# Performance work log

Hardware: AMD Instinct MI355X
Metric: run time of the kernel (lower is better)

The kernel has to match this reference:

```python
import jax, jax.numpy as jnp
import numpy as np

B, T, V, E, H, M, U, W = 8, 64, 30000, 256, 512, 512, 32, 512


def setup_inputs():
    rng = np.random.RandomState(0)
    ks = jax.random.split(jax.random.key(0), 20)
    u_len = rng.randint(U // 2, U + 1, size=B).astype(np.int32)
    w_len = rng.randint(W // 2, W + 1, size=B).astype(np.int32)
    # word2utt[b, j] = utterance index owning word j; padded words -> last valid utt
    w2u = np.zeros((B, W), np.int32)
    for b in range(B):
        j = np.minimum(np.arange(W), w_len[b] - 1)
        w2u[b] = np.minimum((j * u_len[b]) // w_len[b], u_len[b] - 1)
    s = 0.02
    p = lambda i, shp: jax.random.normal(ks[i], shp, jnp.float32) * s
    emb = p(0, (V, E)).at[0].set(0.0)  # padding_idx=0
    return {
        'target': jax.random.randint(ks[1], (B, T), 0, V, jnp.int32),
        'u_output': jax.random.normal(ks[2], (B, U, M), jnp.float32),
        'w_output': jax.random.normal(ks[3], (B, W, M), jnp.float32),
        'u_len': jnp.asarray(u_len), 'w_len': jnp.asarray(w_len), 'word2utt': jnp.asarray(w2u),
        'emb': emb,
        'W_ih': p(4, (3 * H, E)), 'W_hh': p(5, (3 * H, H)),
        'b_ih': p(6, (3 * H,)), 'b_hh': p(7, (3 * H,)),
        'Wu': p(8, (H, M)), 'bu': p(9, (H,)),
        'Ww': p(10, (H, M)), 'bw': p(11, (H,)),
        'Wo': p(12, (V, H + M)), 'bo': p(13, (V,)),
        'Wd': p(14, (1, V)), 'Wy': p(15, (1, E)),
        'Ws': p(16, (1, H)), 'bs': p(17, (1,)),
    }


def reference(target, u_output, w_output, u_len, w_len, word2utt,
              emb, W_ih, W_hh, b_ih, b_hh, Wu, bu, Ww, bw, Wo, bo, Wd, Wy, Ws, bs):
    Bn = target.shape[0]
    Un = u_output.shape[1]
    Vn = Wo.shape[0]
    Au = jnp.einsum('bum,hm->buh', u_output, Wu) + bu  # attention_u(u_output)
    Aw = jnp.einsum('bwm,hm->bwh', w_output, Ww) + bw  # attention_w(w_output)
    u_mask = jnp.arange(Un)[None, :] < u_len[:, None]               # [B,U]
    w_mask = jnp.arange(w_output.shape[1])[None, :] < w_len[:, None]  # [B,W]
    # initial hidden = last valid utterance state (mem_hidden == dec_hidden)
    h0 = jnp.take_along_axis(u_output, (u_len - 1)[:, None, None], axis=1)[:, 0, :]

    def gru_step(x, h):
        gi = x @ W_ih.T + b_ih
        gh = h @ W_hh.T + b_hh
        ir, iz, inn = jnp.split(gi, 3, axis=-1)
        hr, hz, hn = jnp.split(gh, 3, axis=-1)
        r = jax.nn.sigmoid(ir + hr)
        z = jax.nn.sigmoid(iz + hz)
        n = jnp.tanh(inn + r * hn)
        return (1.0 - z) * n + z * h

    def seg_softmax(sw, seg, valid):  # per-batch ragged per-utterance softmax over words
        swm = jnp.where(valid, sw, -jnp.inf)
        m = jax.ops.segment_max(swm, seg, num_segments=Un)
        e = jnp.where(valid, jnp.exp(sw - m[seg]), 0.0)
        d = jax.ops.segment_sum(e, seg, num_segments=Un)
        return e / d[seg]

    def step(carry, yt):
        h, d_prev, eu_prev = carry
        y = emb[yt]                               # [B,E]
        h_new = gru_step(y, h)                    # rnn_output == new hidden (1 layer)
        su = jnp.einsum('bh,buh->bu', h_new, Au)
        su = jax.nn.softmax(jnp.where(u_mask, su, -jnp.inf), axis=-1)
        gamma = jax.nn.sigmoid(d_prev @ Wd.T + y @ Wy.T + h_new @ Ws.T + bs)  # [B,1]
        su = (1.0 - gamma) * su + gamma * eu_prev
        su = su / jnp.sum(su, axis=-1, keepdims=True)
        sw = jnp.einsum('bh,bwh->bw', h_new, Aw)
        pw = jax.vmap(seg_softmax)(sw, word2utt, w_mask)        # [B,W]
        suw = jnp.take_along_axis(su, word2utt, axis=1) * pw    # [B,W]
        ctx = jnp.einsum('bw,bwm->bm', suw, w_output)
        logits = jnp.concatenate([ctx, h_new], axis=-1) @ Wo.T + bo
        dt = jax.nn.log_softmax(logits, axis=-1)
        return (h_new, dt, su), (dt, suw, su)

    init = (h0, jnp.zeros((Bn, Vn), jnp.float32), jnp.zeros((Bn, Un), jnp.float32))
    _, (dts, suws, sus) = jax.lax.scan(step, init, target.T)
    dec_output = jnp.swapaxes(dts, 0, 1)   # [B,T,V]
    scores_uw = jnp.swapaxes(suws, 0, 1)   # [B,T,W]
    scores_u = jnp.swapaxes(sus, 0, 1)     # [B,T,U]
    return dec_output, scores_uw, scores_u
```

## Files before the change

### kernel.cpp

```cpp
#include <hip/hip_runtime.h>
#include <math.h>

typedef unsigned short ushort_t;
typedef unsigned int uint_t;
typedef unsigned long long ulong_t;
typedef __attribute__((ext_vector_type(8))) short s16x8;
typedef __attribute__((ext_vector_type(4))) float f32x4;

#define BB 8
#define TT 64
#define VV 30000
#define VP 30080
#define EE 256
#define HH 512
#define MM 512
#define UU 32
#define WW 512
#define G3 1536
#define NLB 235
#define NDB 235
#define NBG 64

#define OFF_GI    0
#define OFF_YALL  786432
#define OFF_WY    917504
#define OFF_H0    918016
#define OFF_HALL  922112
#define OFF_HU    1184256
#define OFF_HW    1446400
#define OFF_HS    1708544
#define OFF_HWV   1709056
#define OFF_P     1709568
#define OFF_SW    1725952
#define OFF_C     1988096
#define OFF_E     6182400
#define OFF_WV    6198784
#define OFF_PART  6204416
#define OFF_LSE   6208832
#define OFF_WOV   6209344
#define OFF_HBT   13909824
#define OFF_SYNC  14040896

#define DEC_SZ (BB*TT*VV)
#define SUW_OFF DEC_SZ
#define SU_OFF  (DEC_SZ + BB*TT*WW)

__device__ __forceinline__ float sigm(float x){ return 1.0f/(1.0f+__expf(-x)); }
__device__ __forceinline__ ushort_t to_bf16(float f){
  uint_t u = __float_as_uint(f);
  return (ushort_t)((u + 0x7fffu + ((u>>16)&1u)) >> 16);
}
__device__ __forceinline__ float from_bf16(ushort_t s){
  return __uint_as_float(((uint_t)s) << 16);
}


template<int TRANSB>
__global__ void __launch_bounds__(256)
k_gemm_b(const float* __restrict__ A, int lda, int aS,
         const float* __restrict__ B, int ldb, int bS,
         const float* __restrict__ bias,
         float* __restrict__ C, int ldc, int cS, int K){
  A += (size_t)blockIdx.z * aS;
  B += (size_t)blockIdx.z * bS;
  C += (size_t)blockIdx.z * cS;
  __shared__ float As[32][65];
  __shared__ float Bs[32][65];
  int tid = threadIdx.x;
  int bx = blockIdx.x, by = blockIdx.y;
  int tx = tid & 15, ty = tid >> 4;
  float acc[4][4] = {};
  for (int k0 = 0; k0 < K; k0 += 32){
    {
      int r = tid >> 2, cbase = (tid & 3) * 8;
      const float* ap = A + (size_t)(by*64 + r)*lda + k0 + cbase;
      #pragma unroll
      for (int i=0;i<8;++i) As[cbase+i][r] = ap[i];
    }
    if (TRANSB){
      int r = tid >> 2, cbase = (tid & 3) * 8;
      const float* bp = B + (size_t)(bx*64 + r)*ldb + k0 + cbase;
      #pragma unroll
      for (int i=0;i<8;++i) Bs[cbase+i][r] = bp[i];
    } else {
      int kk = tid >> 3, cbase = (tid & 7) * 8;
      const float* bp = B + (size_t)(k0 + kk)*ldb + bx*64 + cbase;
      #pragma unroll
      for (int i=0;i<8;++i) Bs[kk][cbase+i] = bp[i];
    }
    __syncthreads();
    #pragma unroll
    for (int kk=0;kk<32;++kk){
      float a0=As[kk][ty*4+0], a1=As[kk][ty*4+1], a2=As[kk][ty*4+2], a3=As[kk][ty*4+3];
      float b0=Bs[kk][tx*4+0], b1=Bs[kk][tx*4+1], b2=Bs[kk][tx*4+2], b3=Bs[kk][tx*4+3];
      acc[0][0]+=a0*b0; acc[0][1]+=a0*b1; acc[0][2]+=a0*b2; acc[0][3]+=a0*b3;
      acc[1][0]+=a1*b0; acc[1][1]+=a1*b1; acc[1][2]+=a1*b2; acc[1][3]+=a1*b3;
      acc[2][0]+=a2*b0; acc[2][1]+=a2*b1; acc[2][2]+=a2*b2; acc[2][3]+=a2*b3;
      acc[3][0]+=a3*b0; acc[3][1]+=a3*b1; acc[3][2]+=a3*b2; acc[3][3]+=a3*b3;
    }
    __syncthreads();
  }
  #pragma unroll
  for (int i=0;i<4;++i){
    int row = by*64 + ty*4 + i;
    #pragma unroll
    for (int j=0;j<4;++j){
      int col = bx*64 + tx*4 + j;
      float v = acc[i][j];
      if (bias) v += bias[col];
      C[(size_t)row*ldc + col] = v;
    }
  }
}

__global__ void k_gather_y(const int* __restrict__ target, const float* __restrict__ emb,
                           float* __restrict__ ws){
  int idx = blockIdx.x*256 + threadIdx.x;
  int bt = idx >> 8; int e = idx & 255;
  int tok = target[bt];
  ws[OFF_YALL + idx] = emb[tok*EE + e];
}

__global__ void k_wy(const float* __restrict__ Wy, float* __restrict__ ws){
  int wid  = blockIdx.x*4 + (threadIdx.x>>6);
  int lane = threadIdx.x & 63;
  const float* y = ws + OFF_YALL + wid*EE;
  float acc = 0.f;
  for (int e=lane; e<EE; e+=64) acc += y[e]*Wy[e];
  for (int off=32; off; off>>=1) acc += __shfl_xor(acc, off);
  if (lane == 0) ws[OFF_WY + wid] = acc;
}

__global__ void k_h0(const float* __restrict__ u_output, const int* __restrict__ u_len,
                     float* __restrict__ ws){
  int idx = blockIdx.x*256 + threadIdx.x;
  int b = idx >> 9; int k = idx & 511;
  int u = u_len[b]-1;
  ws[OFF_H0 + idx] = u_output[(b*UU+u)*MM + k];
}

__global__ void __launch_bounds__(256)
k_wovc(const float* __restrict__ Wo, ushort_t* __restrict__ wov){
  int idx8 = blockIdx.x*256 + threadIdx.x;
  int v = idx8 >> 6;
  int k8 = (idx8 & 63) << 3;
  uint_t u0=0,u1=0,u2=0,u3=0;
  if (v < VV){
    const float* src = Wo + (size_t)v*1024 + k8;
    float4 f0 = *(const float4*)src;
    float4 f1 = *(const float4*)(src+4);
    u0 = (uint_t)to_bf16(f0.x) | ((uint_t)to_bf16(f0.y) << 16);
    u1 = (uint_t)to_bf16(f0.z) | ((uint_t)to_bf16(f0.w) << 16);
    u2 = (uint_t)to_bf16(f1.x) | ((uint_t)to_bf16(f1.y) << 16);
    u3 = (uint_t)to_bf16(f1.z) | ((uint_t)to_bf16(f1.w) << 16);
  }
  uint4 pk = make_uint4(u0,u1,u2,u3);
  *(uint4*)(wov + (size_t)idx8*8) = pk;
}

__global__ void __launch_bounds__(256)
k_wv(const float* __restrict__ Wo, const float* __restrict__ bo,
     const float* __restrict__ Wd, float* __restrict__ wv){
  __shared__ float wds[128];
  __shared__ float red[256];
  int tid = threadIdx.x;
  int v0 = blockIdx.x*128;
  float pbo=0.f, pwd=0.f;
  if (tid < 128){
    int v = v0 + tid;
    float wd = (v<VV)? Wd[v] : 0.f;
    wds[tid] = wd;
    pbo = wd * ((v<VV)? bo[v] : 0.f);
    pwd = wd;
  }
  __syncthreads();
  float4 acc = {0,0,0,0};
  int nmax = (v0 + 128 <= VV) ? 128 : (VV - v0);
  for (int i=0;i<nmax;++i){
    float wd = wds[i];
    float4 w4 = *(const float4*)(Wo + (size_t)(v0+i)*1024 + tid*4);
    acc.x += wd*w4.x; acc.y += wd*w4.y; acc.z += wd*w4.z; acc.w += wd*w4.w;
  }
  atomicAdd(&wv[tid*4+0], acc.x);
  atomicAdd(&wv[tid*4+1], acc.y);
  atomicAdd(&wv[tid*4+2], acc.z);
  atomicAdd(&wv[tid*4+3], acc.w);
  red[tid] = pbo; __syncthreads();
  for (int s=128; s; s>>=1){ if (tid<s) red[tid]+=red[tid+s]; __syncthreads(); }
  if (tid==0) atomicAdd(&wv[1024], red[0]);
  __syncthreads();
  red[tid] = pwd; __syncthreads();
  for (int s=128; s; s>>=1){ if (tid<s) red[tid]+=red[tid+s]; __syncthreads(); }
  if (tid==0) atomicAdd(&wv[1025], red[0]);
}


__global__ void __launch_bounds__(512)
k_gru_persist(const float* __restrict__ W_hh, const float* __restrict__ b_hh,
              float* __restrict__ ws){
  uint_t* sy    = (uint_t*)(ws + OFF_SYNC);
  uint_t* flags = sy;
  uint_t* go    = sy + 4096;
  int k    = blockIdx.x*8 + (threadIdx.x>>6);
  int lane = threadIdx.x & 63;
  const float* gi_all = ws + OFF_GI;
  const float* wr = W_hh + (size_t)k*HH;
  const float* wz = W_hh + (size_t)(HH+k)*HH;
  const float* wn = W_hh + (size_t)(2*HH+k)*HH;
  float bhr = b_hh[k], bhz = b_hh[HH+k], bhn = b_hh[2*HH+k];

  for (int t=0; t<TT; ++t){
    const float* hin = (t==0) ? (ws+OFF_H0) : (ws+OFF_HALL + (size_t)(t-1)*4096);
    float* hout = ws + OFF_HALL + (size_t)t*4096;
    float pr[8], pz[8], pn[8];
    #pragma unroll
    for (int b=0;b<8;++b){ pr[b]=0.f; pz[b]=0.f; pn[b]=0.f; }
    #pragma unroll 2
    for (int kk=lane; kk<HH; kk+=64){
      float w1 = wr[kk], w2 = wz[kk], w3 = wn[kk];
      #pragma unroll
      for (int b=0;b<8;++b){
        float hv = hin[b*HH+kk];
        pr[b] += hv*w1; pz[b] += hv*w2; pn[b] += hv*w3;
      }
    }
    #pragma unroll
    for (int off=32; off; off>>=1){
      #pragma unroll
      for (int b=0;b<8;++b){
        pr[b] += __shfl_xor(pr[b],off);
        pz[b] += __shfl_xor(pz[b],off);
        pn[b] += __shfl_xor(pn[b],off);
      }
    }
    if (lane == 0){
      #pragma unroll
      for (int b=0;b<8;++b){
        const float* gi = gi_all + (b*TT + t)*G3;
        float r = sigm(gi[k]      + pr[b] + bhr);
        float z = sigm(gi[HH+k]   + pz[b] + bhz);
        float n = tanhf(gi[2*HH+k] + r*(pn[b] + bhn));
        hout[b*HH+k] = (1.f-z)*n + z*hin[b*HH+k];
      }
    }
    __syncthreads();
    if (threadIdx.x == 0)
      __hip_atomic_store(&flags[blockIdx.x*32], (uint_t)(t+1), __ATOMIC_RELEASE, __HIP_MEMORY_SCOPE_AGENT);
    if (blockIdx.x == 0){
      if ((int)threadIdx.x < NBG){
        while (__hip_atomic_load(&flags[threadIdx.x*32], __ATOMIC_RELAXED, __HIP_MEMORY_SCOPE_AGENT) < (uint_t)(t+1))
          __builtin_amdgcn_s_sleep(2);
      }
      __syncthreads();
      if (threadIdx.x == 0)
        __hip_atomic_store(go, (uint_t)(t+1), __ATOMIC_RELEASE, __HIP_MEMORY_SCOPE_AGENT);
    } else {
      if (threadIdx.x == 0){
        while (__hip_atomic_load(go, __ATOMIC_RELAXED, __HIP_MEMORY_SCOPE_AGENT) < (uint_t)(t+1))
          __builtin_amdgcn_s_sleep(2);
      }
    }
    __syncthreads();
  }
}


__global__ void k_hbt(const float* __restrict__ ws, ushort_t* __restrict__ hbt){
  int idx = blockIdx.x*256 + threadIdx.x;
  hbt[idx] = to_bf16(ws[OFF_HALL + idx]);
}

__global__ void __launch_bounds__(256)
k_lh_mfma(const float* __restrict__ Wo, const float* __restrict__ bo,
          const ushort_t* __restrict__ hbt, float* __restrict__ out){
  int tid = threadIdx.x;
  int wv = tid >> 6, l = tid & 63;
  int lm = l & 15, lg = l >> 4;
  int vbase = blockIdx.x*128 + wv*32;
  int rbase = blockIdx.y*128;
  f32x4 acc[2][8];
  #pragma unroll
  for (int s=0;s<2;++s)
    #pragma unroll
    for (int rt=0;rt<8;++rt) acc[s][rt] = (f32x4){0.f,0.f,0.f,0.f};

  for (int k0 = 0; k0 < 512; k0 += 32){
    int kk = k0 + lg*8;
    union { uint_t u[4]; s16x8 s; } af[2];
    #pragma unroll
    for (int s=0;s<2;++s){
      int v = vbase + s*16 + lm; if (v >= VV) v = VV-1;
      const float* ap = Wo + (size_t)v*1024 + 512 + kk;
      float4 f0 = *(const float4*)ap;
      float4 f1 = *(const float4*)(ap+4);
      af[s].u[0] = ((__float_as_uint(f0.x)+0x8000u)>>16) | ((__float_as_uint(f0.y)+0x8000u) & 0xffff0000u);
      af[s].u[1] = ((__float_as_uint(f0.z)+0x8000u)>>16) | ((__float_as_uint(f0.w)+0x8000u) & 0xffff0000u);
      af[s].u[2] = ((__float_as_uint(f1.x)+0x8000u)>>16) | ((__float_as_uint(f1.y)+0x8000u) & 0xffff0000u);
      af[s].u[3] = ((__float_as_uint(f1.z)+0x8000u)>>16) | ((__float_as_uint(f1.w)+0x8000u) & 0xffff0000u);
    }
    #pragma unroll
    for (int rt=0;rt<8;++rt){
      const ushort_t* bp = hbt + (size_t)(rbase + rt*16 + lm)*HH + kk;
      s16x8 bf = *(const s16x8*)bp;
      acc[0][rt] = __builtin_amdgcn_mfma_f32_16x16x32_bf16(af[0].s, bf, acc[0][rt], 0, 0, 0);
      acc[1][rt] = __builtin_amdgcn_mfma_f32_16x16x32_bf16(af[1].s, bf, acc[1][rt], 0, 0, 0);
    }
  }
  float bv[2][4];
  #pragma unroll
  for (int s=0;s<2;++s)
    #pragma unroll
    for (int r=0;r<4;++r){
      int v = vbase + s*16 + lg*4 + r;
      bv[s][r] = (v < VV) ? bo[v] : 0.f;
    }
  #pragma unroll
  for (int rt=0;rt<8;++rt){
    int row = rbase + rt*16 + lm;
    float* orow = out + (size_t)((row&7)*TT + (row>>3))*VV;
    #pragma unroll
    for (int s=0;s<2;++s){
      #pragma unroll
      for (int r=0;r<4;++r){
        int v = vbase + s*16 + lg*4 + r;
        if (v < VV) orow[v] = acc[s][rt][r] + bv[s][r];
      }
    }
  }
}


__global__ void k_hdots(const float* __restrict__ Ws, float* __restrict__ ws){
  int wid  = blockIdx.x*4 + (threadIdx.x>>6);
  int lane = threadIdx.x & 63;
  int row = wid >> 1, which = wid & 1;
  const float* h = ws + OFF_HALL + row*HH;
  const float* src = which ? (ws + OFF_WV + 512) : Ws;
  float acc = 0.f;
  for (int k=lane; k<HH; k+=64) acc += h[k]*src[k];
  for (int off=32; off; off>>=1) acc += __shfl_xor(acc, off);
  if (lane == 0) (which ? ws+OFF_HWV : ws+OFF_HS)[row] = acc;
}

__global__ void k_p(const float* __restrict__ u_output, const int* __restrict__ u_len,
                    float* __restrict__ ws){
  int row = blockIdx.x;
  int b = row & 7;
  int tid = threadIdx.x;
  __shared__ float su_s[UU];
  {
    int u = tid >> 3, l8 = tid & 7;
    const float* hu = ws + OFF_HU + row*512;
    const float* uo = u_output + (size_t)(b*UU + u)*MM;
    float acc = 0.f;
    for (int m=l8; m<MM; m+=8) acc += hu[m]*uo[m];
    acc += __shfl_xor(acc,1); acc += __shfl_xor(acc,2); acc += __shfl_xor(acc,4);
    if (l8 == 0) su_s[u] = acc;
  }
  __syncthreads();
  if (tid < 32){
    int ul = u_len[b];
    float sv = su_s[tid];
    bool valid = tid < ul;
    float mv = valid ? sv : -1e30f;
    for (int off=16; off; off>>=1) mv = fmaxf(mv, __shfl_xor(mv, off));
    float e = valid ? __expf(sv - mv) : 0.f;
    float ssum = e;
    for (int off=16; off; off>>=1) ssum += __shfl_xor(ssum, off);
    ws[OFF_P + row*UU + tid] = e/ssum;
  }
}

__global__ void k_pw(const int* __restrict__ word2utt, const int* __restrict__ w_len,
                     float* __restrict__ ws){
  int row = blockIdx.x;
  int b = row & 7;
  int tid = threadIdx.x;
  __shared__ float sarr[WW];
  __shared__ int   seg[WW];
  __shared__ float marr[UU], darr[UU];
  int wl = w_len[b];
  float* swrow = ws + OFF_SW + row*WW;
  for (int w=tid; w<WW; w+=256){ sarr[w] = swrow[w]; seg[w] = word2utt[b*WW+w]; }
  __syncthreads();
  {
    int g = tid>>3, l8 = tid&7;
    float mv = -1e30f;
    for (int w=l8; w<wl; w+=8) if (seg[w]==g) mv = fmaxf(mv, sarr[w]);
    mv = fmaxf(mv, __shfl_xor(mv,1)); mv = fmaxf(mv, __shfl_xor(mv,2)); mv = fmaxf(mv, __shfl_xor(mv,4));
    float d = 0.f;
    for (int w=l8; w<wl; w+=8) if (seg[w]==g) d += __expf(sarr[w]-mv);
    d += __shfl_xor(d,1); d += __shfl_xor(d,2); d += __shfl_xor(d,4);
    if (l8 == 0){ marr[g]=mv; darr[g]=d; }
  }
  __syncthreads();
  for (int w=tid; w<WW; w+=256){
    float val = 0.f;
    if (w < wl){ int u = seg[w]; val = __expf(sarr[w]-marr[u])/darr[u]; }
    swrow[w] = val;
  }
}

__global__ void __launch_bounds__(256)
k_C(const float* __restrict__ w_output, const int* __restrict__ w_len,
    const int* __restrict__ u_len, const int* __restrict__ word2utt,
    float* __restrict__ ws){
  int row = blockIdx.x;
  int b = row & 7;
  int tid = threadIdx.x;
  __shared__ float pws[WW];
  __shared__ int   seg[WW];
  __shared__ int   st[UU], en[UU];
  __shared__ float wvs[512];
  __shared__ float red4[8];
  int wl = w_len[b], ul = u_len[b];
  const float* pwrow = ws + OFF_SW + row*WW;
  for (int w=tid; w<WW; w+=256){ pws[w] = pwrow[w]; seg[w] = word2utt[b*WW+w]; }
  for (int m=tid; m<512; m+=256) wvs[m] = ws[OFF_WV + m];
  if (tid < UU){ st[tid]=0; en[tid]=0; }
  __syncthreads();
  for (int w=tid; w<wl; w+=256){
    int s = seg[w];
    if (w==0 || seg[w-1]!=s) st[s]=w;
    if (w==wl-1 || seg[w+1]!=s) en[s]=w+1;
  }
  __syncthreads();
  ushort_t* Cu = (ushort_t*)(ws + OFF_C);
  int m0 = tid, m1 = tid + 256;
  int lane = tid & 63, wvi = tid >> 6;
  for (int u=0; u<UU; ++u){
    float acc0=0.f, acc1=0.f;
    if (u < ul){
      int s = st[u], e = en[u];
      for (int w=s; w<e; ++w){
        float p = pws[w];
        const float* wo = w_output + ((size_t)(b*WW+w))*MM;
        acc0 += p*wo[m0];
        acc1 += p*wo[m1];
      }
    }
    size_t cbase = ((size_t)row*UU + u)*512;
    Cu[cbase + m0] = to_bf16(acc0);
    Cu[cbase + m1] = to_bf16(acc1);
    float part = acc0*wvs[m0] + acc1*wvs[m1];
    for (int off=32; off; off>>=1) part += __shfl_xor(part, off);
    if (lane == 0) red4[wvi] = part;
    __syncthreads();
    if (tid == 0) ws[OFF_E + row*UU + u] = red4[0]+red4[1]+red4[2]+red4[3];
    __syncthreads();
  }
}


__global__ void __launch_bounds__(256)
k_decode_persist(const int* __restrict__ u_len, const float* __restrict__ bs,
                 const ushort_t* __restrict__ wov,
                 float* __restrict__ ws, float* __restrict__ out){
  int bid = blockIdx.x;
  int tid = threadIdx.x;
  uint_t* sy    = (uint_t*)(ws + OFF_SYNC);
  uint_t* flags = sy + 8192;
  uint_t* go    = sy + 16000;
  __shared__ float suL[8][32];
  __shared__ float qbufL[8], lseL[8], gamL[8];
  __shared__ int   ulS[8];
  __shared__ uint_t cbU[16*260];
  __shared__ float2 wred[4][8];
  __shared__ float cst[4];
  if (tid == 0){ cst[0]=bs[0]; cst[1]=ws[OFF_WV+1024]; cst[2]=ws[OFF_WV+1025]; }
  if (tid < 8){ qbufL[tid]=0.f; lseL[tid]=0.f; ulS[tid]=u_len[tid]; }
  suL[tid>>5][tid&31] = 0.f;
  for (int i=tid; i<8*260; i+=256) cbU[8*260 + i] = 0u;
  __syncthreads();

  const ulong_t* partq = (const ulong_t*)(ws + OFF_PART);
  int wv = tid >> 6, l = tid & 63;
  int lm = l & 15, lgp = l >> 4;

  for (int t=0; t<TT; ++t){
    int b = tid >> 5, j = tid & 31;
    int row = t*8 + b;

    if (t > 0 && tid < 8)
      lseL[tid] = __hip_atomic_load((const float*)(ws + OFF_LSE + (t-1)*8 + tid),
                                    __ATOMIC_RELAXED, __HIP_MEMORY_SCOPE_AGENT);
    __syncthreads();
    if (tid < 8){
      float pd = 0.f;
      if (t > 0)
        pd = qbufL[tid] + ws[OFF_HWV + (t-1)*8 + tid] + cst[1] - lseL[tid]*cst[2];
      gamL[tid] = sigm(pd + ws[OFF_WY + tid*TT + t] + ws[OFF_HS + t*8 + tid] + cst[0]);
    }
    __syncthreads();
    {
      float gg = gamL[b];
      float p = ws[OFF_P + row*UU + j];
      float eu = suL[b][j];
      float mix = (1.f-gg)*p + gg*eu;
      float s2 = mix;
      #pragma unroll
      for (int off=16; off; off>>=1) s2 += __shfl_xor(s2, off);
      float su = mix / s2;
      suL[b][j] = su;
      float qp = su * ws[OFF_E + row*UU + j];
      #pragma unroll
      for (int off=16; off; off>>=1) qp += __shfl_xor(qp, off);
      if (j == 0) qbufL[b] = qp;
    }
    __syncthreads();
    if (bid < 8 && tid < 32)
      out[SU_OFF + (bid*TT + t)*UU + tid] = suL[bid][tid];
    {
      int m16 = j * 16;
      int ul = ulS[b];
      const ushort_t* Crow = (const ushort_t*)(ws + OFF_C) + ((size_t)row*UU)*512 + m16;
      float acc[16];
      #pragma unroll
      for (int i=0;i<16;++i) acc[i]=0.f;
      for (int u=0; u<ul; ++u){
        float su = suL[b][u];
        uint4 c0 = *(const uint4*)(Crow + (size_t)u*512);
        uint4 c1 = *(const uint4*)(Crow + (size_t)u*512 + 8);
        uint_t cc[8] = {c0.x,c0.y,c0.z,c0.w,c1.x,c1.y,c1.z,c1.w};
        #pragma unroll
        for (int q=0;q<8;++q){
          acc[2*q]   += su * __uint_as_float((cc[q] & 0xffffu) << 16);
          acc[2*q+1] += su * __uint_as_float((cc[q] >> 16) << 16);
        }
      }
      #pragma unroll
      for (int q=0;q<8;++q){
        uint_t pk = (uint_t)to_bf16(acc[2*q]) | ((uint_t)to_bf16(acc[2*q+1]) << 16);
        cbU[b*260 + j*8 + q] = pk;
      }
    }
    __syncthreads();

    {
      int v0w = bid*128 + wv*32;
      f32x4 acc0 = {0.f,0.f,0.f,0.f}, acc1 = {0.f,0.f,0.f,0.f};
      const ushort_t* ap0 = wov + (size_t)(v0w + lm)*512 + lgp*8;
      const ushort_t* ap1 = ap0 + 16*512;
      const uint_t* cbrow = cbU + lm*260 + lgp*4;
      #pragma unroll
      for (int ks=0; ks<16; ++ks){
        s16x8 av0 = *(const s16x8*)(ap0 + ks*32);
        s16x8 av1 = *(const s16x8*)(ap1 + ks*32);
        s16x8 bv  = *(const s16x8*)(cbrow + ks*16);
        acc0 = __builtin_amdgcn_mfma_f32_16x16x32_bf16(av0, bv, acc0, 0, 0, 0);
        acc1 = __builtin_amdgcn_mfma_f32_16x16x32_bf16(av1, bv, acc1, 0, 0, 0);
      }
      float pm = -1e30f, ps = 0.f;
      if (lm < 8){
        float* orow = out + ((size_t)(lm*TT + t))*VV;
        float l8v[8];
        #pragma unroll
        for (int vt=0; vt<2; ++vt){
          int vb = v0w + vt*16 + lgp*4;
          f32x4 a = vt ? acc1 : acc0;
          if (vb + 3 < VV){
            float4 o = *(const float4*)(orow + vb);
            float g0 = a[0]+o.x, g1 = a[1]+o.y, g2 = a[2]+o.z, g3 = a[3]+o.w;
            *(float4*)(orow + vb) = make_float4(g0,g1,g2,g3);
            l8v[vt*4+0]=g0; l8v[vt*4+1]=g1; l8v[vt*4+2]=g2; l8v[vt*4+3]=g3;
          } else {
            #pragma unroll
            for (int r=0;r<4;++r){
              int v = vb + r;
              float g = -1e30f;
              if (v < VV){ g = a[r] + orow[v]; orow[v] = g; }
              l8v[vt*4+r] = g;
            }
          }
        }
        #pragma unroll
        for (int i=0;i<8;++i) pm = fmaxf(pm, l8v[i]);
        #pragma unroll
        for (int i=0;i<8;++i) ps += (l8v[i] > -5e29f) ? __expf(l8v[i]-pm) : 0.f;
      }
      #pragma unroll
      for (int off=16; off<=32; off<<=1){
        float mo = __shfl_xor(pm, off);
        float so = __shfl_xor(ps, off);
        float nm = fmaxf(pm, mo);
        ps = ps*__expf(pm-nm) + so*__expf(mo-nm);
        pm = nm;
      }
      if (lgp == 0 && lm < 8) wred[wv][lm] = make_float2(pm, ps);
    }
    __syncthreads();
    if (tid < 8){
      float m = -1e30f, s = 0.f;
      #pragma unroll
      for (int w=0; w<4; ++w){
        float2 e = wred[w][tid];
        float nm = fmaxf(m, e.x);
        s = s*__expf(m-nm) + e.y*__expf(e.x-nm);
        m = nm;
      }
      *(float2*)(ws + OFF_PART + bid*16 + tid*2) = make_float2(m, s);
    }

    __syncthreads();
    if (tid == 0)
      __hip_atomic_store(&flags[bid*32], (uint_t)(t+1), __ATOMIC_RELEASE, __HIP_MEMORY_SCOPE_AGENT);
    if (bid == 0){
      if (tid < NDB){
        while (__hip_atomic_load(&flags[tid*32], __ATOMIC_RELAXED, __HIP_MEMORY_SCOPE_AGENT) < (uint_t)(t+1))
          __builtin_amdgcn_s_sleep(2);
      }
      __syncthreads();
      {
        float ma = -1e30f, sa = 0.f;
        for (int i=j; i<NLB; i+=32){
          ulong_t pq = __hip_atomic_load(&partq[i*8 + b], __ATOMIC_RELAXED, __HIP_MEMORY_SCOPE_AGENT);
          float m = __uint_as_float((uint_t)pq);
          float s = __uint_as_float((uint_t)(pq >> 32));
          float mm = fmaxf(ma, m);
          sa = sa*__expf(ma-mm) + s*__expf(m-mm);
          ma = mm;
        }
        #pragma unroll
        for (int off=16; off; off>>=1){
          float mo = __shfl_xor(ma, off);
          float so = __shfl_xor(sa, off);
          float mm = fmaxf(ma, mo);
          sa = sa*__expf(ma-mm) + so*__expf(mo-mm);
          ma = mm;
        }
        if (j == 0) ws[OFF_LSE + t*8 + b] = ma + logf(sa);
      }
      __syncthreads();
      if (tid == 0)
        __hip_atomic_store(go, (uint_t)(t+1), __ATOMIC_RELEASE, __HIP_MEMORY_SCOPE_AGENT);
    } else {
      if (tid == 0){
        while (__hip_atomic_load(go, __ATOMIC_RELAXED, __HIP_MEMORY_SCOPE_AGENT) < (uint_t)(t+1))
          __builtin_amdgcn_s_sleep(2);
      }
    }
    __syncthreads();
  }
}


__global__ void k_sub2(const float* __restrict__ ws, float* __restrict__ out){
  int v = blockIdx.x*256 + threadIdx.x;
  int tb = blockIdx.y;
  int t = tb >> 3, b = tb & 7;
  if (v < VV) out[(size_t)(b*TT+t)*VV + v] -= ws[OFF_LSE + tb];
}

__global__ void k_suw2(const int* __restrict__ word2utt, const float* __restrict__ ws,
                       float* __restrict__ out){
  int row = blockIdx.x;
  int t = row >> 3, b = row & 7;
  int tid = threadIdx.x;
  for (int w=tid; w<WW; w+=256){
    int seg = word2utt[b*WW + w];
    float su = out[SU_OFF + (b*TT+t)*UU + seg];
    float pw = ws[OFF_SW + row*WW + w];
    out[SUW_OFF + (b*TT+t)*WW + w] = su*pw;
  }
}

extern "C" void kernel_launch(void* const* d_in, const int* in_sizes, int n_in,
                              void* d_out, int out_size, void* d_ws, size_t ws_size,
                              hipStream_t stream) {
  const int*   target   = (const int*)d_in[0];
  const float* u_output = (const float*)d_in[1];
  const float* w_output = (const float*)d_in[2];
  const int*   u_len    = (const int*)d_in[3];
  const int*   w_len    = (const int*)d_in[4];
  const int*   word2utt = (const int*)d_in[5];
  const float* emb      = (const float*)d_in[6];
  const float* W_ih     = (const float*)d_in[7];
  const float* W_hh     = (const float*)d_in[8];
  const float* b_ih     = (const float*)d_in[9];
  const float* b_hh     = (const float*)d_in[10];
  const float* Wu       = (const float*)d_in[11];
  const float* Ww       = (const float*)d_in[13];
  const float* Wo       = (const float*)d_in[15];
  const float* bo       = (const float*)d_in[16];
  const float* Wd       = (const float*)d_in[17];
  const float* Wy       = (const float*)d_in[18];
  const float* Ws       = (const float*)d_in[19];
  const float* bs       = (const float*)d_in[20];
  float* out = (float*)d_out;
  float* ws  = (float*)d_ws;
  ushort_t* wov = (ushort_t*)(ws + OFF_WOV);
  ushort_t* hbt = (ushort_t*)(ws + OFF_HBT);

  hipMemsetAsync(ws + OFF_SYNC, 0, 16384*sizeof(float), stream);

  hipLaunchKernelGGL(k_gather_y, dim3(512), dim3(256), 0, stream, target, emb, ws);
  hipLaunchKernelGGL((k_gemm_b<1>), dim3(24,8,1), dim3(256), 0, stream,
                     ws+OFF_YALL, 256, 0, W_ih, 256, 0, b_ih, ws+OFF_GI, 1536, 0, 256);
  hipLaunchKernelGGL(k_wy, dim3(128), dim3(256), 0, stream, Wy, ws);
  hipLaunchKernelGGL(k_h0, dim3(16), dim3(256), 0, stream, u_output, u_len, ws);
  hipLaunchKernelGGL(k_wovc, dim3(7520), dim3(256), 0, stream, Wo, wov);
  hipMemsetAsync(ws + OFF_WV, 0, 1536*sizeof(float), stream);
  hipLaunchKernelGGL(k_wv, dim3(NLB), dim3(256), 0, stream, Wo, bo, Wd, ws+OFF_WV);

  hipLaunchKernelGGL(k_gru_persist, dim3(NBG), dim3(512), 0, stream, W_hh, b_hh, ws);

  hipLaunchKernelGGL(k_hbt, dim3(1024), dim3(256), 0, stream, ws, hbt);
  hipLaunchKernelGGL(k_lh_mfma, dim3(235, 4), dim3(256), 0, stream, Wo, bo, hbt, out);
  hipLaunchKernelGGL((k_gemm_b<0>), dim3(8,8,1), dim3(256), 0, stream,
                     ws+OFF_HALL, 512, 0, Wu, 512, 0, (const float*)nullptr, ws+OFF_HU, 512, 0, 512);
  hipLaunchKernelGGL((k_gemm_b<0>), dim3(8,8,1), dim3(256), 0, stream,
                     ws+OFF_HALL, 512, 0, Ww, 512, 0, (const float*)nullptr, ws+OFF_HW, 512, 0, 512);
  hipLaunchKernelGGL(k_hdots, dim3(256), dim3(256), 0, stream, Ws, ws);
  hipLaunchKernelGGL(k_p, dim3(512), dim3(256), 0, stream, u_output, u_len, ws);
  hipLaunchKernelGGL((k_gemm_b<1>), dim3(8,1,8), dim3(256), 0, stream,
                     ws+OFF_HW, 4096, 512, w_output, 512, 262144, (const float*)nullptr,
                     ws+OFF_SW, 4096, 512, 512);
  hipLaunchKernelGGL(k_pw, dim3(512), dim3(256), 0, stream, word2utt, w_len, ws);
  hipLaunchKernelGGL(k_C, dim3(512), dim3(256), 0, stream,
                     w_output, w_len, u_len, word2utt, ws);

  hipLaunchKernelGGL(k_decode_persist, dim3(NDB), dim3(256), 0, stream,
                     u_len, bs, wov, ws, out);

  hipLaunchKernelGGL(k_sub2, dim3(118, 512), dim3(256), 0, stream, ws, out);
  hipLaunchKernelGGL(k_suw2, dim3(512), dim3(256), 0, stream, word2utt, ws, out);
}
```

Baseline: 2.122 ms.

## Shrink persistent decode grid to 64 blocks of 1024 threads

Restructures the persistent decode kernel from 235 blocks of 256 threads to 64 blocks of 1024 threads, each block covering 512 vocab rows with 16 waves. The padded bf16 Wo copy grows to a 32768-row buffer, so the workspace offsets move and the conversion kernel gets more blocks. The per-step context mix is redistributed so all 1024 threads each handle 4 columns. The final log-sum-exp reduction becomes one 64-lane wave reduction per batch row. Fewer blocks mean cheaper grid-wide flag polling and barrier work each step, at the cost of more serial work per block and heavier intra-block syncs.

After: 2.537 ms. 19.5% more time.

```diff
diff --git a/kernel.cpp b/kernel.cpp
--- a/kernel.cpp
+++ b/kernel.cpp
@@ -11,6 +11,7 @@
 #define TT 64
 #define VV 30000
 #define VP 30080
+#define VPW 32768
 #define EE 256
 #define HH 512
 #define MM 512
@@ -18,7 +19,7 @@
 #define WW 512
 #define G3 1536
 #define NLB 235
-#define NDB 235
+#define NDB 64
 #define NBG 64
 
 #define OFF_GI    0
@@ -38,8 +39,8 @@
 #define OFF_PART  6204416
 #define OFF_LSE   6208832
 #define OFF_WOV   6209344
-#define OFF_HBT   13909824
-#define OFF_SYNC  14040896
+#define OFF_HBT   14597952
+#define OFF_SYNC  14729024
 
 #define DEC_SZ (BB*TT*VV)
 #define SUW_OFF DEC_SZ
@@ -452,7 +453,7 @@
 }
 
 
-__global__ void __launch_bounds__(256)
+__global__ void __launch_bounds__(1024)
 k_decode_persist(const int* __restrict__ u_len, const float* __restrict__ bs,
                  const ushort_t* __restrict__ wov,
                  float* __restrict__ ws, float* __restrict__ out){
@@ -465,22 +466,19 @@
   __shared__ float qbufL[8], lseL[8], gamL[8];
   __shared__ int   ulS[8];
   __shared__ uint_t cbU[16*260];
-  __shared__ float2 wred[4][8];
+  __shared__ float2 wred[16][8];
   __shared__ float cst[4];
   if (tid == 0){ cst[0]=bs[0]; cst[1]=ws[OFF_WV+1024]; cst[2]=ws[OFF_WV+1025]; }
   if (tid < 8){ qbufL[tid]=0.f; lseL[tid]=0.f; ulS[tid]=u_len[tid]; }
-  suL[tid>>5][tid&31] = 0.f;
-  for (int i=tid; i<8*260; i+=256) cbU[8*260 + i] = 0u;
+  if (tid < 256) suL[tid>>5][tid&31] = 0.f;
+  for (int i=tid; i<8*260; i+=1024) cbU[8*260 + i] = 0u;
   __syncthreads();
 
   const ulong_t* partq = (const ulong_t*)(ws + OFF_PART);
-  int wv = tid >> 6, l = tid & 63;
+  int wid = tid >> 6, l = tid & 63;
   int lm = l & 15, lgp = l >> 4;
 
   for (int t=0; t<TT; ++t){
-    int b = tid >> 5, j = tid & 31;
-    int row = t*8 + b;
-
     if (t > 0 && tid < 8)
       lseL[tid] = __hip_atomic_load((const float*)(ws + OFF_LSE + (t-1)*8 + tid),
                                     __ATOMIC_RELAXED, __HIP_MEMORY_SCOPE_AGENT);
@@ -492,7 +490,9 @@
       gamL[tid] = sigm(pd + ws[OFF_WY + tid*TT + t] + ws[OFF_HS + t*8 + tid] + cst[0]);
     }
     __syncthreads();
-    {
+    if (tid < 256){
+      int b = tid >> 5, j = tid & 31;
+      int row = t*8 + b;
       float gg = gamL[b];
       float p = ws[OFF_P + row*UU + j];
       float eu = suL[b][j];
@@ -511,33 +511,27 @@
     if (bid < 8 && tid < 32)
       out[SU_OFF + (bid*TT + t)*UU + tid] = suL[bid][tid];
     {
-      int m16 = j * 16;
-      int ul = ulS[b];
-      const ushort_t* Crow = (const ushort_t*)(ws + OFF_C) + ((size_t)row*UU)*512 + m16;
-      float acc[16];
-      #pragma unroll
-      for (int i=0;i<16;++i) acc[i]=0.f;
+      int cb = tid >> 7, mq = tid & 127;
+      int m0 = mq * 4;
+      int row = t*8 + cb;
+      int ul = ulS[cb];
+      const ushort_t* Crow = (const ushort_t*)(ws + OFF_C) + ((size_t)row*UU)*512 + m0;
+      float a0=0.f, a1=0.f, a2=0.f, a3=0.f;
       for (int u=0; u<ul; ++u){
-        float su = suL[b][u];
-        uint4 c0 = *(const uint4*)(Crow + (size_t)u*512);
-        uint4 c1 = *(const uint4*)(Crow + (size_t)u*512 + 8);
-        uint_t cc[8] = {c0.x,c0.y,c0.z,c0.w,c1.x,c1.y,c1.z,c1.w};
-        #pragma unroll
-        for (int q=0;q<8;++q){
-          acc[2*q]   += su * __uint_as_float((cc[q] & 0xffffu) << 16);
-          acc[2*q+1] += su * __uint_as_float((cc[q] >> 16) << 16);
-        }
-      }
-      #pragma unroll
-      for (int q=0;q<8;++q){
-        uint_t pk = (uint_t)to_bf16(acc[2*q]) | ((uint_t)to_bf16(acc[2*q+1]) << 16);
-        cbU[b*260 + j*8 + q] = pk;
-      }
+        float su = suL[cb][u];
+        uint2 cc = *(const uint2*)(Crow + (size_t)u*512);
+        a0 += su * __uint_as_float((cc.x & 0xffffu) << 16);
+        a1 += su * __uint_as_float((cc.x >> 16) << 16);
+        a2 += su * __uint_as_float((cc.y & 0xffffu) << 16);
+        a3 += su * __uint_as_float((cc.y >> 16) << 16);
+      }
+      cbU[cb*260 + mq*2]     = (uint_t)to_bf16(a0) | ((uint_t)to_bf16(a1) << 16);
+      cbU[cb*260 + mq*2 + 1] = (uint_t)to_bf16(a2) | ((uint_t)to_bf16(a3) << 16);
     }
     __syncthreads();
 
     {
-      int v0w = bid*128 + wv*32;
+      int v0w = bid*512 + wid*32;
       f32x4 acc0 = {0.f,0.f,0.f,0.f}, acc1 = {0.f,0.f,0.f,0.f};
       const ushort_t* ap0 = wov + (size_t)(v0w + lm)*512 + lgp*8;
       const ushort_t* ap1 = ap0 + 16*512;
@@ -586,13 +580,13 @@
         ps = ps*__expf(pm-nm) + so*__expf(mo-nm);
         pm = nm;
       }
-      if (lgp == 0 && lm < 8) wred[wv][lm] = make_float2(pm, ps);
+      if (lgp == 0 && lm < 8) wred[wid][lm] = make_float2(pm, ps);
     }
     __syncthreads();
     if (tid < 8){
       float m = -1e30f, s = 0.f;
       #pragma unroll
-      for (int w=0; w<4; ++w){
+      for (int w=0; w<16; ++w){
         float2 e = wred[w][tid];
         float nm = fmaxf(m, e.x);
         s = s*__expf(m-nm) + e.y*__expf(e.x-nm);
@@ -610,25 +604,21 @@
           __builtin_amdgcn_s_sleep(2);
       }
       __syncthreads();
-      {
-        float ma = -1e30f, sa = 0.f;
-        for (int i=j; i<NLB; i+=32){
-          ulong_t pq = __hip_atomic_load(&partq[i*8 + b], __ATOMIC_RELAXED, __HIP_MEMORY_SCOPE_AGENT);
-          float m = __uint_as_float((uint_t)pq);
-          float s = __uint_as_float((uint_t)(pq >> 32));
-          float mm = fmaxf(ma, m);
-          sa = sa*__expf(ma-mm) + s*__expf(m-mm);
-          ma = mm;
-        }
+      if (wid < 8){
+        ulong_t pq = __hip_atomic_load(&partq[l*8 + wid], __ATOMIC_RELAXED, __HIP_MEMORY_SCOPE_AGENT);
+        float ma = __uint_as_float((uint_t)pq);
+        float sa = __uint_as_float((uint_t)(pq >> 32));
         #pragma unroll
-        for (int off=16; off; off>>=1){
+        for (int off=32; off; off>>=1){
           float mo = __shfl_xor(ma, off);
           float so = __shfl_xor(sa, off);
           float mm = fmaxf(ma, mo);
           sa = sa*__expf(ma-mm) + so*__expf(mo-mm);
           ma = mm;
         }
-        if (j == 0) ws[OFF_LSE + t*8 + b] = ma + logf(sa);
+        if (l == 0)
+          __hip_atomic_store((float*)(ws + OFF_LSE + t*8 + wid), ma + logf(sa),
+                             __ATOMIC_RELAXED, __HIP_MEMORY_SCOPE_AGENT);
       }
       __syncthreads();
       if (tid == 0)
@@ -698,7 +688,7 @@
                      ws+OFF_YALL, 256, 0, W_ih, 256, 0, b_ih, ws+OFF_GI, 1536, 0, 256);
   hipLaunchKernelGGL(k_wy, dim3(128), dim3(256), 0, stream, Wy, ws);
   hipLaunchKernelGGL(k_h0, dim3(16), dim3(256), 0, stream, u_output, u_len, ws);
-  hipLaunchKernelGGL(k_wovc, dim3(7520), dim3(256), 0, stream, Wo, wov);
+  hipLaunchKernelGGL(k_wovc, dim3(8192), dim3(256), 0, stream, Wo, wov);
   hipMemsetAsync(ws + OFF_WV, 0, 1536*sizeof(float), stream);
   hipLaunchKernelGGL(k_wv, dim3(NLB), dim3(256), 0, stream, Wo, bo, Wd, ws+OFF_WV);
 
@@ -719,7 +709,7 @@
   hipLaunchKernelGGL(k_C, dim3(512), dim3(256), 0, stream,
                      w_output, w_len, u_len, word2utt, ws);
 
-  hipLaunchKernelGGL(k_decode_persist, dim3(NDB), dim3(256), 0, stream,
+  hipLaunchKernelGGL(k_decode_persist, dim3(NDB), dim3(1024), 0, stream,
                      u_len, bs, wov, ws, out);
 
   hipLaunchKernelGGL(k_sub2, dim3(118, 512), dim3(256), 0, stream, ws, out);
```

## Replace centralized grid barriers with all-poll flags and distributed LSE reduction

Applied to the files above, without the earlier changes.

In the GRU persistent kernel, every block now polls all peer flags directly instead of waiting on a master block that then publishes a go flag, which removes one hop of cross-block latency per step. The bf16 conversion of hidden states is folded into the GRU kernel's tail, dropping a separate launch. In the decode kernel, eight blocks each reduce the log-sum-exp for one batch row in parallel, using double-buffered partials and per-row completion flags, instead of block 0 reducing everything serially. The trade-off is more polling traffic on the flag lines, plus a tree reduction in shared memory.

After: 2.072 ms. 2.4% less time.

```diff
diff --git a/kernel.cpp b/kernel.cpp
--- a/kernel.cpp
+++ b/kernel.cpp
@@ -17,7 +17,6 @@
 #define UU 32
 #define WW 512
 #define G3 1536
-#define NLB 235
 #define NDB 235
 #define NBG 64
 
@@ -35,11 +34,11 @@
 #define OFF_C     1988096
 #define OFF_E     6182400
 #define OFF_WV    6198784
-#define OFF_PART  6204416
-#define OFF_LSE   6208832
-#define OFF_WOV   6209344
-#define OFF_HBT   13909824
-#define OFF_SYNC  14040896
+#define OFF_PART  6200320
+#define OFF_LSE   6208512
+#define OFF_WOV   6209024
+#define OFF_HBT   13909504
+#define OFF_SYNC  14040576
 
 #define DEC_SZ (BB*TT*VV)
 #define SUW_OFF DEC_SZ
@@ -49,9 +48,6 @@
 __device__ __forceinline__ ushort_t to_bf16(float f){
   uint_t u = __float_as_uint(f);
   return (ushort_t)((u + 0x7fffu + ((u>>16)&1u)) >> 16);
-}
-__device__ __forceinline__ float from_bf16(ushort_t s){
-  return __uint_as_float(((uint_t)s) << 16);
 }
 
 
@@ -198,9 +194,7 @@
 __global__ void __launch_bounds__(512)
 k_gru_persist(const float* __restrict__ W_hh, const float* __restrict__ b_hh,
               float* __restrict__ ws){
-  uint_t* sy    = (uint_t*)(ws + OFF_SYNC);
-  uint_t* flags = sy;
-  uint_t* go    = sy + 4096;
+  uint_t* flags = (uint_t*)(ws + OFF_SYNC);
   int k    = blockIdx.x*8 + (threadIdx.x>>6);
   int lane = threadIdx.x & 63;
   const float* gi_all = ws + OFF_GI;
@@ -246,29 +240,20 @@
     __syncthreads();
     if (threadIdx.x == 0)
       __hip_atomic_store(&flags[blockIdx.x*32], (uint_t)(t+1), __ATOMIC_RELEASE, __HIP_MEMORY_SCOPE_AGENT);
-    if (blockIdx.x == 0){
-      if ((int)threadIdx.x < NBG){
-        while (__hip_atomic_load(&flags[threadIdx.x*32], __ATOMIC_RELAXED, __HIP_MEMORY_SCOPE_AGENT) < (uint_t)(t+1))
-          __builtin_amdgcn_s_sleep(2);
-      }
-      __syncthreads();
-      if (threadIdx.x == 0)
-        __hip_atomic_store(go, (uint_t)(t+1), __ATOMIC_RELEASE, __HIP_MEMORY_SCOPE_AGENT);
-    } else {
-      if (threadIdx.x == 0){
-        while (__hip_atomic_load(go, __ATOMIC_RELAXED, __HIP_MEMORY_SCOPE_AGENT) < (uint_t)(t+1))
-          __builtin_amdgcn_s_sleep(2);
-      }
-    }
-    __syncthreads();
-  }
-}
-
-
-__global__ void k_hbt(const float* __restrict__ ws, ushort_t* __restrict__ hbt){
-  int idx = blockIdx.x*256 + threadIdx.x;
-  hbt[idx] = to_bf16(ws[OFF_HALL + idx]);
-}
+    if ((int)threadIdx.x < NBG){
+      while (__hip_atomic_load(&flags[threadIdx.x*32], __ATOMIC_RELAXED, __HIP_MEMORY_SCOPE_AGENT) < (uint_t)(t+1))
+        __builtin_amdgcn_s_sleep(1);
+    }
+    __syncthreads();
+  }
+  {
+    ushort_t* hbt = (ushort_t*)(ws + OFF_HBT);
+    int base = (blockIdx.x*512 + threadIdx.x)*8;
+    #pragma unroll
+    for (int i=0;i<8;++i) hbt[base+i] = to_bf16(ws[OFF_HALL + base + i]);
+  }
+}
+
 
 __global__ void __launch_bounds__(256)
 k_lh_mfma(const float* __restrict__ Wo, const float* __restrict__ bo,
@@ -458,14 +443,15 @@
                  float* __restrict__ ws, float* __restrict__ out){
   int bid = blockIdx.x;
   int tid = threadIdx.x;
-  uint_t* sy    = (uint_t*)(ws + OFF_SYNC);
-  uint_t* flags = sy + 8192;
-  uint_t* go    = sy + 16000;
+  uint_t* sy     = (uint_t*)(ws + OFF_SYNC);
+  uint_t* flags  = sy + 8192;
+  uint_t* flags2 = sy + 16000;
   __shared__ float suL[8][32];
   __shared__ float qbufL[8], lseL[8], gamL[8];
   __shared__ int   ulS[8];
   __shared__ uint_t cbU[16*260];
   __shared__ float2 wred[4][8];
+  __shared__ float smr[256], ssr[256];
   __shared__ float cst[4];
   if (tid == 0){ cst[0]=bs[0]; cst[1]=ws[OFF_WV+1024]; cst[2]=ws[OFF_WV+1025]; }
   if (tid < 8){ qbufL[tid]=0.f; lseL[tid]=0.f; ulS[tid]=u_len[tid]; }
@@ -473,7 +459,6 @@
   for (int i=tid; i<8*260; i+=256) cbU[8*260 + i] = 0u;
   __syncthreads();
 
-  const ulong_t* partq = (const ulong_t*)(ws + OFF_PART);
   int wv = tid >> 6, l = tid & 63;
   int lm = l & 15, lgp = l >> 4;
 
@@ -598,46 +583,47 @@
         s = s*__expf(m-nm) + e.y*__expf(e.x-nm);
         m = nm;
       }
-      *(float2*)(ws + OFF_PART + bid*16 + tid*2) = make_float2(m, s);
+      *(float2*)(ws + OFF_PART + (t&1)*4096 + (bid*8 + tid)*2) = make_float2(m, s);
     }
 
     __syncthreads();
     if (tid == 0)
       __hip_atomic_store(&flags[bid*32], (uint_t)(t+1), __ATOMIC_RELEASE, __HIP_MEMORY_SCOPE_AGENT);
-    if (bid == 0){
+    if (bid < 8){
       if (tid < NDB){
         while (__hip_atomic_load(&flags[tid*32], __ATOMIC_RELAXED, __HIP_MEMORY_SCOPE_AGENT) < (uint_t)(t+1))
           __builtin_amdgcn_s_sleep(2);
       }
       __syncthreads();
       {
-        float ma = -1e30f, sa = 0.f;
-        for (int i=j; i<NLB; i+=32){
-          ulong_t pq = __hip_atomic_load(&partq[i*8 + b], __ATOMIC_RELAXED, __HIP_MEMORY_SCOPE_AGENT);
-          float m = __uint_as_float((uint_t)pq);
-          float s = __uint_as_float((uint_t)(pq >> 32));
-          float mm = fmaxf(ma, m);
-          sa = sa*__expf(ma-mm) + s*__expf(m-mm);
-          ma = mm;
+        const ulong_t* partq = (const ulong_t*)(ws + OFF_PART + (t&1)*4096);
+        float m = -1e30f, s = 0.f;
+        if (tid < NDB){
+          ulong_t pq = __hip_atomic_load(&partq[tid*8 + bid], __ATOMIC_RELAXED, __HIP_MEMORY_SCOPE_AGENT);
+          m = __uint_as_float((uint_t)pq);
+          s = __uint_as_float((uint_t)(pq >> 32));
         }
-        #pragma unroll
-        for (int off=16; off; off>>=1){
-          float mo = __shfl_xor(ma, off);
-          float so = __shfl_xor(sa, off);
-          float mm = fmaxf(ma, mo);
-          sa = sa*__expf(ma-mm) + so*__expf(mo-mm);
-          ma = mm;
+        smr[tid]=m; ssr[tid]=s; __syncthreads();
+        for (int st=128; st; st>>=1){
+          if (tid < st){
+            float m1 = smr[tid], s1 = ssr[tid];
+            float m2 = smr[tid+st], s2 = ssr[tid+st];
+            float mm = fmaxf(m1, m2);
+            ssr[tid] = s1*__expf(m1-mm) + s2*__expf(m2-mm);
+            smr[tid] = mm;
+          }
+          __syncthreads();
         }
-        if (j == 0) ws[OFF_LSE + t*8 + b] = ma + logf(sa);
-      }
-      __syncthreads();
-      if (tid == 0)
-        __hip_atomic_store(go, (uint_t)(t+1), __ATOMIC_RELEASE, __HIP_MEMORY_SCOPE_AGENT);
-    } else {
-      if (tid == 0){
-        while (__hip_atomic_load(go, __ATOMIC_RELAXED, __HIP_MEMORY_SCOPE_AGENT) < (uint_t)(t+1))
-          __builtin_amdgcn_s_sleep(2);
-      }
+        if (tid == 0){
+          __hip_atomic_store((float*)(ws + OFF_LSE + t*8 + bid), smr[0] + logf(ssr[0]),
+                             __ATOMIC_RELAXED, __HIP_MEMORY_SCOPE_AGENT);
+          __hip_atomic_store(&flags2[bid*32], (uint_t)(t+1), __ATOMIC_RELEASE, __HIP_MEMORY_SCOPE_AGENT);
+        }
+      }
+    }
+    if (tid < 8){
+      while (__hip_atomic_load(&flags2[tid*32], __ATOMIC_RELAXED, __HIP_MEMORY_SCOPE_AGENT) < (uint_t)(t+1))
+        __builtin_amdgcn_s_sleep(1);
     }
     __syncthreads();
   }
@@ -700,11 +686,10 @@
   hipLaunchKernelGGL(k_h0, dim3(16), dim3(256), 0, stream, u_output, u_len, ws);
   hipLaunchKernelGGL(k_wovc, dim3(7520), dim3(256), 0, stream, Wo, wov);
   hipMemsetAsync(ws + OFF_WV, 0, 1536*sizeof(float), stream);
-  hipLaunchKernelGGL(k_wv, dim3(NLB), dim3(256), 0, stream, Wo, bo, Wd, ws+OFF_WV);
+  hipLaunchKernelGGL(k_wv, dim3(235), dim3(256), 0, stream, Wo, bo, Wd, ws+OFF_WV);
 
   hipLaunchKernelGGL(k_gru_persist, dim3(NBG), dim3(512), 0, stream, W_hh, b_hh, ws);
 
-  hipLaunchKernelGGL(k_hbt, dim3(1024), dim3(256), 0, stream, ws, hbt);
   hipLaunchKernelGGL(k_lh_mfma, dim3(235, 4), dim3(256), 0, stream, Wo, bo, hbt, out);
   hipLaunchKernelGGL((k_gemm_b<0>), dim3(8,8,1), dim3(256), 0, stream,
                      ws+OFF_HALL, 512, 0, Wu, 512, 0, (const float*)nullptr, ws+OFF_HU, 512, 0, 512);
```
